# Optimization experiments

Measured on AMD Instinct MI355X. Metric: run time of the kernel, lower is better.

Reference implementation:

```python
import jax, jax.numpy as jnp
import numpy as np

EPS = 1e-5


def setup_inputs() -> dict:
    key = jax.random.key(0)
    ks = jax.random.split(key, 8)
    B, S, D, H, IN, OUT = 4096, 128, 64, 256, 8192, 1
    s = lambda n: 1.0 / np.sqrt(n)
    return {
        "x": jax.random.normal(ks[0], (B, IN), dtype=jnp.float32),
        "gamma": jnp.ones((IN,), jnp.float32),
        "beta": jnp.zeros((IN,), jnp.float32),
        "W_in": jax.random.normal(ks[1], (IN, IN), jnp.float32) * s(IN),
        "W_ih": jax.random.normal(ks[2], (4 * H, D), jnp.float32) * s(H),
        "b_ih": jnp.zeros((4 * H,), jnp.float32),
        "W_hh": jax.random.normal(ks[3], (4 * H, H), jnp.float32) * s(H),
        "b_hh": jnp.zeros((4 * H,), jnp.float32),
        "W_ta": jax.random.normal(ks[4], (S, S * H), jnp.float32) * s(S * H),
        "b_ta": jnp.zeros((S,), jnp.float32),
        "W_out": jax.random.normal(ks[5], (OUT, H), jnp.float32) * s(H),
    }


def _ta_lstm(x, gamma, beta, W_in, W_ih, b_ih, W_hh, b_hh, W_ta, b_ta, W_out):
    B, IN = x.shape
    H4 = W_hh.shape[0]
    H = H4 // 4
    S = W_ta.shape[0]
    D = IN // S

    # BatchNorm1d (training mode: batch statistics, biased variance)
    mean = jnp.mean(x, axis=0)
    var = jnp.mean(jnp.square(x - mean), axis=0)
    xn = (x - mean) * jax.lax.rsqrt(var + EPS) * gamma + beta

    # layer_in (no bias)
    proj = xn @ W_in.T  # [B, IN]

    # precompute input-side gate activations for all timesteps at once
    xs = proj.reshape(B, S, D)  # time-major column blocks
    gates_x = jnp.einsum("bsd,gd->sbg", xs, W_ih) + b_ih + b_hh  # [S, B, 4H]

    def step(carry, gx):
        h, c = carry
        gates = gx + h @ W_hh.T  # [B, 4H]
        i, f, g, o = jnp.split(gates, 4, axis=-1)
        i = jax.nn.sigmoid(i)
        f = jax.nn.sigmoid(f)
        g = jnp.tanh(g)
        o = jax.nn.sigmoid(o)
        c = f * c + i * g
        h = o * jnp.tanh(c)
        return (h, c), h

    h0 = jnp.zeros((B, H), x.dtype)
    c0 = jnp.zeros((B, H), x.dtype)
    _, hs = jax.lax.scan(step, (h0, c0), gates_x)  # hs: [S, B, H]

    hs_bsh = jnp.transpose(hs, (1, 0, 2))  # [B, S, H]
    total_ht = hs_bsh.reshape(B, S * H)  # matches torch.cat over time

    # temporal attention: relu -> softmax over last dim
    beta_t = jax.nn.softmax(jax.nn.relu(total_ht @ W_ta.T + b_ta), axis=-1)  # [B, S]

    pooled = jnp.einsum("bsh,bs->bh", hs_bsh, beta_t)  # [B, H]
    return pooled @ W_out.T  # [B, out_dim]


def reference(x, gamma, beta, W_in, W_ih, b_ih, W_hh, b_hh, W_ta, b_ta, W_out):
    return _ta_lstm(x, gamma, beta, W_in, W_ih, b_ih, W_hh, b_hh, W_ta, b_ta, W_out)
```

## Files before the change

kernel.cpp:

```cpp
#include <hip/hip_runtime.h>
#include <hip/hip_bf16.h>

#define BB 4096
#define INF 8192
#define SS 128
#define HH 256

typedef __attribute__((ext_vector_type(8))) short short8;
typedef __attribute__((ext_vector_type(4))) float f32x4;

__device__ __forceinline__ float sigm(float x) { return 1.f / (1.f + __expf(-x)); }
__device__ __forceinline__ float tanh_fast(float x) {
    float cx = fminf(15.f, fmaxf(-15.f, x));
    float e = __expf(2.f * cx);
    return (e - 1.f) / (e + 1.f);
}
__device__ __forceinline__ unsigned short f2bf(float f) {
    __hip_bfloat16 b = __float2bfloat16(f);
    return *(unsigned short*)&b;
}
__device__ __forceinline__ float bf2f(unsigned short u) {
    __hip_bfloat16 b = *(__hip_bfloat16*)&u;
    return __bfloat162float(b);
}

#define GLD(g, l) __builtin_amdgcn_global_load_lds(                              \
        (const __attribute__((address_space(1))) void*)(g),                      \
        (__attribute__((address_space(3))) void*)(l), 16, 0, 0)

__global__ __launch_bounds__(256) void bn_partial(const float* __restrict__ x,
                                                  float* __restrict__ colsum,
                                                  float* __restrict__ colsumsq) {
    int j = blockIdx.x * 256 + threadIdx.x;
    int r0 = blockIdx.y * 256;
    float s1 = 0.f, s2 = 0.f;
    for (int r = r0; r < r0 + 256; ++r) {
        float v = x[(size_t)r * INF + j];
        s1 += v;
        s2 += v * v;
    }
    atomicAdd(&colsum[j], s1);
    atomicAdd(&colsumsq[j], s2);
}

__global__ __launch_bounds__(256) void bn_finalize(const float* __restrict__ colsum,
                                                   const float* __restrict__ colsumsq,
                                                   const float* __restrict__ gamma,
                                                   const float* __restrict__ beta,
                                                   float* __restrict__ scl,
                                                   float* __restrict__ shf) {
    int j = blockIdx.x * 256 + threadIdx.x;
    float mean = colsum[j] * (1.f / BB);
    float var = colsumsq[j] * (1.f / BB) - mean * mean;
    float a = gamma[j] * rsqrtf(var + 1e-5f);
    scl[j] = a;
    shf[j] = beta[j] - mean * a;
}

__global__ __launch_bounds__(256) void split_x(const float* __restrict__ x,
                                               const float* __restrict__ scl,
                                               const float* __restrict__ shf,
                                               unsigned short* __restrict__ hi,
                                               unsigned short* __restrict__ lo) {
    size_t i = ((size_t)blockIdx.x * 256 + threadIdx.x) * 4;
    float4 v = *(const float4*)(x + i);
    int col = (int)(i & (INF - 1));
    float4 s = *(const float4*)(scl + col);
    float4 h = *(const float4*)(shf + col);
    float f[4] = {fmaf(v.x, s.x, h.x), fmaf(v.y, s.y, h.y),
                  fmaf(v.z, s.z, h.z), fmaf(v.w, s.w, h.w)};
    ushort4 hv, lv;
    unsigned short* hp = (unsigned short*)&hv;
    unsigned short* lp = (unsigned short*)&lv;
#pragma unroll
    for (int k = 0; k < 4; ++k) {
        unsigned short hb = f2bf(f[k]);
        hp[k] = hb;
        lp[k] = f2bf(f[k] - bf2f(hb));
    }
    *(ushort4*)(hi + i) = hv;
    *(ushort4*)(lo + i) = lv;
}

__global__ __launch_bounds__(256) void split_w(const float* __restrict__ w,
                                               unsigned short* __restrict__ hi,
                                               unsigned short* __restrict__ lo) {
    size_t i = ((size_t)blockIdx.x * 256 + threadIdx.x) * 4;
    float4 v = *(const float4*)(w + i);
    float f[4] = {v.x, v.y, v.z, v.w};
    ushort4 hv, lv;
    unsigned short* hp = (unsigned short*)&hv;
    unsigned short* lp = (unsigned short*)&lv;
#pragma unroll
    for (int k = 0; k < 4; ++k) {
        unsigned short hb = f2bf(f[k]);
        hp[k] = hb;
        lp[k] = f2bf(f[k] - bf2f(hb));
    }
    *(ushort4*)(hi + i) = hv;
    *(ushort4*)(lo + i) = lv;
}

__global__ __launch_bounds__(128) void pack_w(const float* __restrict__ Wih,
                                              const float* __restrict__ Whh,
                                              const float* __restrict__ bih,
                                              const float* __restrict__ bhh,
                                              unsigned short* __restrict__ Wch,
                                              unsigned short* __restrict__ Wcl,
                                              float* __restrict__ biascat) {
    int r = blockIdx.x;
    int c = r >> 2, g = r & 3;
    int t = threadIdx.x;
    if (t == 0) biascat[r] = bih[g * 256 + c] + bhh[g * 256 + c];
    if (t >= 80) return;
    float4 v;
    if (t < 16)
        v = *(const float4*)(Wih + (size_t)(g * 256 + c) * 64 + t * 4);
    else
        v = *(const float4*)(Whh + (size_t)(g * 256 + c) * 256 + (t - 16) * 4);
    float f[4] = {v.x, v.y, v.z, v.w};
    ushort4 hv, lv;
    unsigned short* hp = (unsigned short*)&hv;
    unsigned short* lp = (unsigned short*)&lv;
#pragma unroll
    for (int k = 0; k < 4; ++k) {
        unsigned short hb = f2bf(f[k]);
        hp[k] = hb;
        lp[k] = f2bf(f[k] - bf2f(hb));
    }
    *(ushort4*)(Wch + (size_t)r * 320 + t * 4) = hv;
    *(ushort4*)(Wcl + (size_t)r * 320 + t * 4) = lv;
}

__global__ __launch_bounds__(256) void gemm_mfma_split(
    const unsigned short* __restrict__ Ah, const unsigned short* __restrict__ Al,
    const unsigned short* __restrict__ Bh, const unsigned short* __restrict__ Bl,
    unsigned short* __restrict__ projsplit, int K) {
    __shared__ unsigned short AsH[4096], AsL[4096], BsH[4096], BsL[4096];
    const int tid = threadIdx.x;
    const int lane = tid & 63, wid = tid >> 6;
    int bid = blockIdx.x;
    int grp = bid >> 8, loc = bid & 255;
    int bx = ((grp & 3) << 4) | (loc & 15);
    int by = ((grp >> 2) << 4) | (loc >> 4);
    const int row0 = by << 7, col0 = bx << 7;
    const int wm = (wid & 1) << 6, wn = (wid >> 1) << 6;
    const int q = lane >> 4, l15 = lane & 15;

    const int s0 = wid * 128 + lane, s1 = s0 + 64;
    const int r0 = s0 >> 2, k0 = (((s0 & 3) ^ ((r0 >> 1) & 3)) << 3);
    const int r1 = s1 >> 2, k1 = (((s1 & 3) ^ ((r1 >> 1) & 3)) << 3);
    const size_t aoff0 = (size_t)(row0 + r0) * K + k0;
    const size_t aoff1 = (size_t)(row0 + r1) * K + k1;
    const size_t boff0 = (size_t)(col0 + r0) * K + k0;
    const size_t boff1 = (size_t)(col0 + r1) * K + k1;
    const int lb0 = (wid * 128) * 8, lb1 = lb0 + 512;

    f32x4 acc[4][4];
#pragma unroll
    for (int i = 0; i < 4; ++i)
#pragma unroll
        for (int j = 0; j < 4; ++j) acc[i][j] = (f32x4){0.f, 0.f, 0.f, 0.f};

    for (int kb = 0; kb < K; kb += 32) {
        __syncthreads();
        GLD(Ah + aoff0 + kb, &AsH[lb0]);
        GLD(Ah + aoff1 + kb, &AsH[lb1]);
        GLD(Al + aoff0 + kb, &AsL[lb0]);
        GLD(Al + aoff1 + kb, &AsL[lb1]);
        GLD(Bh + boff0 + kb, &BsH[lb0]);
        GLD(Bh + boff1 + kb, &BsH[lb1]);
        GLD(Bl + boff0 + kb, &BsL[lb0]);
        GLD(Bl + boff1 + kb, &BsL[lb1]);
        __syncthreads();

        short8 ahf[4], alf[4], bhf[4], blf[4];
#pragma unroll
        for (int i = 0; i < 4; ++i) {
            int ra = wm + i * 16 + l15;
            int offa = ra * 32 + ((q ^ ((ra >> 1) & 3)) << 3);
            ahf[i] = *(const short8*)&AsH[offa];
            alf[i] = *(const short8*)&AsL[offa];
            int rb = wn + i * 16 + l15;
            int offb = rb * 32 + ((q ^ ((rb >> 1) & 3)) << 3);
            bhf[i] = *(const short8*)&BsH[offb];
            blf[i] = *(const short8*)&BsL[offb];
        }
#pragma unroll
        for (int i = 0; i < 4; ++i)
#pragma unroll
            for (int j = 0; j < 4; ++j) {
                acc[i][j] = __builtin_amdgcn_mfma_f32_16x16x32_bf16(ahf[i], bhf[j], acc[i][j], 0, 0, 0);
                acc[i][j] = __builtin_amdgcn_mfma_f32_16x16x32_bf16(ahf[i], blf[j], acc[i][j], 0, 0, 0);
                acc[i][j] = __builtin_amdgcn_mfma_f32_16x16x32_bf16(alf[i], bhf[j], acc[i][j], 0, 0, 0);
            }
    }

#pragma unroll
    for (int i = 0; i < 4; ++i)
#pragma unroll
        for (int j = 0; j < 4; ++j) {
            int col = col0 + wn + j * 16 + l15;
            int slice = col >> 6, c6 = col & 63;
            unsigned short* ps = projsplit + (size_t)slice * 524288;
#pragma unroll
            for (int r = 0; r < 4; ++r) {
                int row = row0 + wm + i * 16 + q * 4 + r;
                float v = acc[i][j][r];
                unsigned short hb = f2bf(v);
                ps[row * 64 + c6] = hb;
                ps[262144 + row * 64 + c6] = f2bf(v - bf2f(hb));
            }
        }
}

__global__ __launch_bounds__(256) void lstm_step_mfma(
    const unsigned short* __restrict__ projsplit,
    const unsigned short* __restrict__ Wch, const unsigned short* __restrict__ Wcl,
    const float* __restrict__ biascat,
    const unsigned short* __restrict__ hin_h, const unsigned short* __restrict__ hin_l,
    unsigned short* __restrict__ hout_h, unsigned short* __restrict__ hout_l,
    float* __restrict__ cbuf, float* __restrict__ hs, int s) {
    __shared__ unsigned short AsH[4096], AsL[4096], BsH[4096], BsL[4096];
    __shared__ float gates[128][132];
    __shared__ float sbias[128];
    const int tid = threadIdx.x;
    const int lane = tid & 63, wid = tid >> 6;
    const int row0 = (blockIdx.x & 31) << 7;
    const int col0 = (blockIdx.x >> 5) << 7;
    if (tid < 128) sbias[tid] = biascat[col0 + tid];

    const int wm = (wid & 1) << 6, wn = (wid >> 1) << 6;
    const int q = lane >> 4, l15 = lane & 15;
    const int s0 = wid * 128 + lane, s1 = s0 + 64;
    const int r0 = s0 >> 2, k0 = (((s0 & 3) ^ ((r0 >> 1) & 3)) << 3);
    const int r1 = s1 >> 2, k1 = (((s1 & 3) ^ ((r1 >> 1) & 3)) << 3);
    const int lb0 = (wid * 128) * 8, lb1 = lb0 + 512;

    const unsigned short* psl = projsplit + (size_t)s * 524288;

    f32x4 acc[4][4];
#pragma unroll
    for (int i = 0; i < 4; ++i)
#pragma unroll
        for (int j = 0; j < 4; ++j) acc[i][j] = (f32x4){0.f, 0.f, 0.f, 0.f};

    for (int kb = 0; kb < 10; ++kb) {
        __syncthreads();
        const unsigned short *pah0, *pal0, *pah1, *pal1;
        if (kb < 2) {
            int off0 = (row0 + r0) * 64 + kb * 32 + k0;
            int off1 = (row0 + r1) * 64 + kb * 32 + k1;
            pah0 = psl + off0;          pal0 = psl + 262144 + off0;
            pah1 = psl + off1;          pal1 = psl + 262144 + off1;
        } else {
            int kh = kb * 32 - 64;
            int off0 = (row0 + r0) * HH + kh + k0;
            int off1 = (row0 + r1) * HH + kh + k1;
            pah0 = hin_h + off0;        pal0 = hin_l + off0;
            pah1 = hin_h + off1;        pal1 = hin_l + off1;
        }
        const unsigned short* pbh0 = Wch + (size_t)(col0 + r0) * 320 + kb * 32 + k0;
        const unsigned short* pbh1 = Wch + (size_t)(col0 + r1) * 320 + kb * 32 + k1;
        const unsigned short* pbl0 = Wcl + (size_t)(col0 + r0) * 320 + kb * 32 + k0;
        const unsigned short* pbl1 = Wcl + (size_t)(col0 + r1) * 320 + kb * 32 + k1;
        GLD(pah0, &AsH[lb0]);
        GLD(pah1, &AsH[lb1]);
        GLD(pal0, &AsL[lb0]);
        GLD(pal1, &AsL[lb1]);
        GLD(pbh0, &BsH[lb0]);
        GLD(pbh1, &BsH[lb1]);
        GLD(pbl0, &BsL[lb0]);
        GLD(pbl1, &BsL[lb1]);
        __syncthreads();

        short8 ahf[4], alf[4], bhf[4], blf[4];
#pragma unroll
        for (int i = 0; i < 4; ++i) {
            int ra = wm + i * 16 + l15;
            int offa = ra * 32 + ((q ^ ((ra >> 1) & 3)) << 3);
            ahf[i] = *(const short8*)&AsH[offa];
            alf[i] = *(const short8*)&AsL[offa];
            int rb = wn + i * 16 + l15;
            int offb = rb * 32 + ((q ^ ((rb >> 1) & 3)) << 3);
            bhf[i] = *(const short8*)&BsH[offb];
            blf[i] = *(const short8*)&BsL[offb];
        }
#pragma unroll
        for (int i = 0; i < 4; ++i)
#pragma unroll
            for (int j = 0; j < 4; ++j) {
                acc[i][j] = __builtin_amdgcn_mfma_f32_16x16x32_bf16(ahf[i], bhf[j], acc[i][j], 0, 0, 0);
                acc[i][j] = __builtin_amdgcn_mfma_f32_16x16x32_bf16(ahf[i], blf[j], acc[i][j], 0, 0, 0);
                acc[i][j] = __builtin_amdgcn_mfma_f32_16x16x32_bf16(alf[i], bhf[j], acc[i][j], 0, 0, 0);
            }
    }

    __syncthreads();
#pragma unroll
    for (int i = 0; i < 4; ++i)
#pragma unroll
        for (int j = 0; j < 4; ++j)
#pragma unroll
            for (int r = 0; r < 4; ++r)
                gates[wm + i * 16 + q * 4 + r][wn + j * 16 + l15] = acc[i][j][r];
    __syncthreads();

    const int hc = tid & 31, rg = tid >> 5;
    const int hbase = col0 >> 2;
#pragma unroll
    for (int rr = 0; rr < 16; ++rr) {
        int row = rg * 16 + rr;
        int b = row0 + row;
        float4 g4 = *(const float4*)&gates[row][4 * hc];
        float4 b4 = *(const float4*)&sbias[4 * hc];
        size_t ci = (size_t)b * HH + hbase + hc;
        float cold = (s > 0) ? cbuf[ci] : 0.f;
        float i_ = sigm(g4.x + b4.x);
        float f_ = sigm(g4.y + b4.y);
        float g_ = tanh_fast(g4.z + b4.z);
        float o_ = sigm(g4.w + b4.w);
        float cn = fmaf(f_, cold, i_ * g_);
        float hn = o_ * tanh_fast(cn);
        cbuf[ci] = cn;
        hs[(size_t)s * (BB * HH) + ci] = hn;
        unsigned short hb = f2bf(hn);
        hout_h[ci] = hb;
        hout_l[ci] = f2bf(hn - bf2f(hb));
    }
}

__global__ __launch_bounds__(256) void q_kernel(const float* __restrict__ hs,
                                                const float* __restrict__ wout,
                                                float* __restrict__ q) {
    int wid = threadIdx.x >> 6, lane = threadIdx.x & 63;
    int p = (blockIdx.x << 2) + wid;
    int b = p & (BB - 1), s = p >> 12;
    const float* hp = hs + ((size_t)s * BB + b) * HH + (lane << 2);
    float4 h4 = *(const float4*)hp;
    float4 w4 = *(const float4*)(wout + (lane << 2));
    float v = h4.x * w4.x + h4.y * w4.y + h4.z * w4.z + h4.w * w4.w;
#pragma unroll
    for (int off = 32; off; off >>= 1) v += __shfl_xor(v, off);
    if (lane == 0) q[b * SS + s] = v;
}

__global__ __launch_bounds__(256) void attn_part(const float* __restrict__ hs,
                                                 const float* __restrict__ Wta,
                                                 float* __restrict__ part) {
    __shared__ float As[16][68];
    __shared__ float Bs[16][132];
    const int tid = threadIdx.x;
    const int tx = tid & 15, ty = tid >> 4;
    const int row0 = blockIdx.x << 6;
    const int jc = blockIdx.y;
    const int lrA = tid >> 2, lkA = (tid & 3) << 2;
    const int lrB = tid >> 1, lkB = (tid & 1) << 3;

    float acc[4][8];
#pragma unroll
    for (int i = 0; i < 4; ++i)
#pragma unroll
        for (int j = 0; j < 8; ++j) acc[i][j] = 0.f;

    for (int kb = 0; kb < 256; ++kb) {
        int k0 = (jc << 12) + (kb << 4);
        int sidx = k0 >> 8, h0 = k0 & 255;
        float4 av = *(const float4*)(hs + ((size_t)sidx * BB + row0 + lrA) * HH + h0 + lkA);
        const float* wp = Wta + (size_t)lrB * (SS * HH) + k0 + lkB;
        float4 bv0 = *(const float4*)wp;
        float4 bv1 = *(const float4*)(wp + 4);
        __syncthreads();
        As[lkA + 0][lrA] = av.x;
        As[lkA + 1][lrA] = av.y;
        As[lkA + 2][lrA] = av.z;
        As[lkA + 3][lrA] = av.w;
        Bs[lkB + 0][lrB] = bv0.x;
        Bs[lkB + 1][lrB] = bv0.y;
        Bs[lkB + 2][lrB] = bv0.z;
        Bs[lkB + 3][lrB] = bv0.w;
        Bs[lkB + 4][lrB] = bv1.x;
        Bs[lkB + 5][lrB] = bv1.y;
        Bs[lkB + 6][lrB] = bv1.z;
        Bs[lkB + 7][lrB] = bv1.w;
        __syncthreads();
#pragma unroll
        for (int k = 0; k < 16; ++k) {
            float4 af = *(const float4*)&As[k][ty << 2];
            float4 b0 = *(const float4*)&Bs[k][tx << 2];
            float4 b1 = *(const float4*)&Bs[k][64 + (tx << 2)];
            float ar[4] = {af.x, af.y, af.z, af.w};
            float br[8] = {b0.x, b0.y, b0.z, b0.w, b1.x, b1.y, b1.z, b1.w};
#pragma unroll
            for (int i = 0; i < 4; ++i)
#pragma unroll
                for (int j = 0; j < 8; ++j)
                    acc[i][j] = fmaf(ar[i], br[j], acc[i][j]);
        }
    }
#pragma unroll
    for (int i = 0; i < 4; ++i) {
        int b = row0 + (ty << 2) + i;
        float* pp = part + ((size_t)jc * BB + b) * SS;
        float4 o0 = {acc[i][0], acc[i][1], acc[i][2], acc[i][3]};
        float4 o1 = {acc[i][4], acc[i][5], acc[i][6], acc[i][7]};
        *(float4*)(pp + (tx << 2)) = o0;
        *(float4*)(pp + 64 + (tx << 2)) = o1;
    }
}

__global__ __launch_bounds__(256) void attn_finalize(const float* __restrict__ part,
                                                     const float* __restrict__ b_ta,
                                                     const float* __restrict__ q,
                                                     float* __restrict__ out) {
    int wid = threadIdx.x >> 6, lane = threadIdx.x & 63;
    int b = (blockIdx.x << 2) + wid;
    float l0 = b_ta[lane], l1 = b_ta[lane + 64];
#pragma unroll
    for (int j = 0; j < 8; ++j) {
        const float* pp = part + ((size_t)j * BB + b) * SS;
        l0 += pp[lane];
        l1 += pp[lane + 64];
    }
    l0 = fmaxf(l0, 0.f);
    l1 = fmaxf(l1, 0.f);
    float mx = fmaxf(l0, l1);
#pragma unroll
    for (int off = 32; off; off >>= 1) mx = fmaxf(mx, __shfl_xor(mx, off));
    float e0 = __expf(l0 - mx), e1 = __expf(l1 - mx);
    float num = fmaf(e0, q[b * SS + lane], e1 * q[b * SS + lane + 64]);
    float den = e0 + e1;
#pragma unroll
    for (int off = 32; off; off >>= 1) {
        num += __shfl_xor(num, off);
        den += __shfl_xor(den, off);
    }
    if (lane == 0) out[b] = num / den;
}

extern "C" void kernel_launch(void* const* d_in, const int* in_sizes, int n_in,
                              void* d_out, int out_size, void* d_ws, size_t ws_size,
                              hipStream_t stream) {
    const float* x     = (const float*)d_in[0];
    const float* gamma = (const float*)d_in[1];
    const float* beta_ = (const float*)d_in[2];
    const float* W_in  = (const float*)d_in[3];
    const float* W_ih  = (const float*)d_in[4];
    const float* b_ih  = (const float*)d_in[5];
    const float* W_hh  = (const float*)d_in[6];
    const float* b_hh  = (const float*)d_in[7];
    const float* W_ta  = (const float*)d_in[8];
    const float* b_ta  = (const float*)d_in[9];
    const float* W_out = (const float*)d_in[10];
    float* out = (float*)d_out;

    float* ws = (float*)d_ws;
    float* colsum   = ws;
    float* colsumsq = ws + 8192;
    float* scl      = ws + 16384;
    float* shf      = ws + 24576;
    float* biascat  = ws + 32768;
    float* qbuf     = ws + 33792;
    float* part     = ws + 558080;
    float* cbuf     = ws + 4752384;
    unsigned short* Wch   = (unsigned short*)(ws + 5800960);
    unsigned short* Wcl   = (unsigned short*)(ws + 5964800);
    unsigned short* hsp0h = (unsigned short*)(ws + 6128640);
    unsigned short* hsp0l = (unsigned short*)(ws + 6652928);
    unsigned short* hsp1h = (unsigned short*)(ws + 7177216);
    unsigned short* hsp1l = (unsigned short*)(ws + 7701504);
    float* hs = ws + 8388608;
    unsigned short* xh = (unsigned short*)hs;
    unsigned short* xl = xh + 33554432;
    unsigned short* Wh = xl + 33554432;
    unsigned short* Wl = Wh + 67108864;
    unsigned short* projsplit = (unsigned short*)(ws + 8388608 + 108003328);

    hipMemsetAsync(colsum, 0, 2 * 8192 * sizeof(float), stream);
    hipMemsetAsync(hsp0h, 0, 4194304, stream);

    bn_partial<<<dim3(32, 16), 256, 0, stream>>>(x, colsum, colsumsq);
    bn_finalize<<<32, 256, 0, stream>>>(colsum, colsumsq, gamma, beta_, scl, shf);
    split_x<<<32768, 256, 0, stream>>>(x, scl, shf, xh, xl);
    split_w<<<65536, 256, 0, stream>>>(W_in, Wh, Wl);
    pack_w<<<1024, 128, 0, stream>>>(W_ih, W_hh, b_ih, b_hh, Wch, Wcl, biascat);
    gemm_mfma_split<<<2048, 256, 0, stream>>>(xh, xl, Wh, Wl, projsplit, INF);
    for (int s = 0; s < 128; ++s) {
        const unsigned short* hih = (s & 1) ? hsp1h : hsp0h;
        const unsigned short* hil = (s & 1) ? hsp1l : hsp0l;
        unsigned short* hoh = (s & 1) ? hsp0h : hsp1h;
        unsigned short* hol = (s & 1) ? hsp0l : hsp1l;
        lstm_step_mfma<<<256, 256, 0, stream>>>(projsplit, Wch, Wcl, biascat,
                                                hih, hil, hoh, hol, cbuf, hs, s);
    }
    q_kernel<<<131072, 256, 0, stream>>>(hs, W_out, qbuf);
    attn_part<<<dim3(64, 8), 256, 0, stream>>>(hs, W_ta, part);
    attn_finalize<<<1024, 256, 0, stream>>>(part, b_ta, qbuf, out);
}
```

Before: 5.472 ms.

## Rewrite split-bf16 input GEMM as 256x256 tile kernel with 4-stage LDS ring pipeline

```diff
diff --git a/kernel.cpp b/kernel.cpp
--- a/kernel.cpp
+++ b/kernel.cpp
@@ -132,86 +132,152 @@
     *(ushort4*)(Wcl + (size_t)r * 320 + t * 4) = lv;
 }
 
-__global__ __launch_bounds__(256) void gemm_mfma_split(
+__global__ __launch_bounds__(512, 2) void gemm8(
     const unsigned short* __restrict__ Ah, const unsigned short* __restrict__ Al,
     const unsigned short* __restrict__ Bh, const unsigned short* __restrict__ Bl,
-    unsigned short* __restrict__ projsplit, int K) {
-    __shared__ unsigned short AsH[4096], AsL[4096], BsH[4096], BsL[4096];
+    unsigned short* __restrict__ projsplit) {
+    __shared__ unsigned short As[32768];
+    __shared__ unsigned short Bs[32768];
     const int tid = threadIdx.x;
     const int lane = tid & 63, wid = tid >> 6;
-    int bid = blockIdx.x;
-    int grp = bid >> 8, loc = bid & 255;
-    int bx = ((grp & 3) << 4) | (loc & 15);
-    int by = ((grp >> 2) << 4) | (loc >> 4);
-    const int row0 = by << 7, col0 = bx << 7;
-    const int wm = (wid & 1) << 6, wn = (wid >> 1) << 6;
-    const int q = lane >> 4, l15 = lane & 15;
-
-    const int s0 = wid * 128 + lane, s1 = s0 + 64;
-    const int r0 = s0 >> 2, k0 = (((s0 & 3) ^ ((r0 >> 1) & 3)) << 3);
-    const int r1 = s1 >> 2, k1 = (((s1 & 3) ^ ((r1 >> 1) & 3)) << 3);
-    const size_t aoff0 = (size_t)(row0 + r0) * K + k0;
-    const size_t aoff1 = (size_t)(row0 + r1) * K + k1;
-    const size_t boff0 = (size_t)(col0 + r0) * K + k0;
-    const size_t boff1 = (size_t)(col0 + r1) * K + k1;
-    const int lb0 = (wid * 128) * 8, lb1 = lb0 + 512;
-
-    f32x4 acc[4][4];
+    const int wmi = wid >> 2, wni = wid & 3;
+    const int l15 = lane & 15, q = lane >> 4;
+
+    const int bid = blockIdx.x;
+    const int wg = ((bid & 7) << 6) | (bid >> 3);
+    const int bx = wg >> 4, by = wg & 15;
+    const int row0 = by << 8, col0 = bx << 8;
+
+    const int slot = (tid & 7) ^ ((tid >> 3) & 7);
+    const int rr = ((tid >> 3) << 1) | (slot >> 2);
+    const int kgo = (slot & 3) << 3;
+    const int wbase = wid << 9;
+
+    const int dsb = ((l15 >> 1) << 6) + (((q | ((l15 & 1) << 2)) ^ (l15 >> 1)) << 3);
+
+#define STAGE_A(srcp, ks, ring)                                                   \
+    do {                                                                          \
+        const unsigned short* _g = (srcp) + (size_t)(row0 + rr) * INF + (ks) + kgo; \
+        GLD(_g, &As[((ring) << 13) + wbase]);                                     \
+        GLD(_g + (size_t)128 * INF, &As[((ring) << 13) + 4096 + wbase]);          \
+    } while (0)
+#define STAGE_B(srcp, ks, ring)                                                   \
+    do {                                                                          \
+        const unsigned short* _g = (srcp) + (size_t)(col0 + rr) * INF + (ks) + kgo; \
+        GLD(_g, &Bs[((ring) << 13) + wbase]);                                     \
+        GLD(_g + (size_t)128 * INF, &Bs[((ring) << 13) + 4096 + wbase]);          \
+    } while (0)
+#define LDA4(d, i2, rgofs)                                                        \
+    do {                                                                          \
+        d[0] = *(const short8*)&As[(rgofs) + wmi * 4096 + (i2)*2048 + 0 * 512 + dsb]; \
+        d[1] = *(const short8*)&As[(rgofs) + wmi * 4096 + (i2)*2048 + 1 * 512 + dsb]; \
+        d[2] = *(const short8*)&As[(rgofs) + wmi * 4096 + (i2)*2048 + 2 * 512 + dsb]; \
+        d[3] = *(const short8*)&As[(rgofs) + wmi * 4096 + (i2)*2048 + 3 * 512 + dsb]; \
+    } while (0)
+#define LDB4(d, rgofs)                                                            \
+    do {                                                                          \
+        d[0] = *(const short8*)&Bs[(rgofs) + wni * 2048 + 0 * 512 + dsb];         \
+        d[1] = *(const short8*)&Bs[(rgofs) + wni * 2048 + 1 * 512 + dsb];         \
+        d[2] = *(const short8*)&Bs[(rgofs) + wni * 2048 + 2 * 512 + dsb];         \
+        d[3] = *(const short8*)&Bs[(rgofs) + wni * 2048 + 3 * 512 + dsb];         \
+    } while (0)
+#define MFMA16(accx)                                                              \
+    do {                                                                          \
+        __builtin_amdgcn_s_setprio(1);                                            \
+        _Pragma("unroll") for (int i_ = 0; i_ < 4; ++i_)                          \
+            _Pragma("unroll") for (int j_ = 0; j_ < 4; ++j_)                      \
+                accx[i_][j_] = __builtin_amdgcn_mfma_f32_16x16x32_bf16(           \
+                    a[i_], b[j_], accx[i_][j_], 0, 0, 0);                         \
+        __builtin_amdgcn_s_setprio(0);                                            \
+    } while (0)
+
+    f32x4 acc0[4][4], acc1[4][4];
 #pragma unroll
     for (int i = 0; i < 4; ++i)
 #pragma unroll
-        for (int j = 0; j < 4; ++j) acc[i][j] = (f32x4){0.f, 0.f, 0.f, 0.f};
-
-    for (int kb = 0; kb < K; kb += 32) {
-        __syncthreads();
-        GLD(Ah + aoff0 + kb, &AsH[lb0]);
-        GLD(Ah + aoff1 + kb, &AsH[lb1]);
-        GLD(Al + aoff0 + kb, &AsL[lb0]);
-        GLD(Al + aoff1 + kb, &AsL[lb1]);
-        GLD(Bh + boff0 + kb, &BsH[lb0]);
-        GLD(Bh + boff1 + kb, &BsH[lb1]);
-        GLD(Bl + boff0 + kb, &BsL[lb0]);
-        GLD(Bl + boff1 + kb, &BsL[lb1]);
-        __syncthreads();
-
-        short8 ahf[4], alf[4], bhf[4], blf[4];
-#pragma unroll
-        for (int i = 0; i < 4; ++i) {
-            int ra = wm + i * 16 + l15;
-            int offa = ra * 32 + ((q ^ ((ra >> 1) & 3)) << 3);
-            ahf[i] = *(const short8*)&AsH[offa];
-            alf[i] = *(const short8*)&AsL[offa];
-            int rb = wn + i * 16 + l15;
-            int offb = rb * 32 + ((q ^ ((rb >> 1) & 3)) << 3);
-            bhf[i] = *(const short8*)&BsH[offb];
-            blf[i] = *(const short8*)&BsL[offb];
+        for (int j = 0; j < 4; ++j) {
+            acc0[i][j] = (f32x4){0.f, 0.f, 0.f, 0.f};
+            acc1[i][j] = (f32x4){0.f, 0.f, 0.f, 0.f};
         }
-#pragma unroll
-        for (int i = 0; i < 4; ++i)
-#pragma unroll
-            for (int j = 0; j < 4; ++j) {
-                acc[i][j] = __builtin_amdgcn_mfma_f32_16x16x32_bf16(ahf[i], bhf[j], acc[i][j], 0, 0, 0);
-                acc[i][j] = __builtin_amdgcn_mfma_f32_16x16x32_bf16(ahf[i], blf[j], acc[i][j], 0, 0, 0);
-                acc[i][j] = __builtin_amdgcn_mfma_f32_16x16x32_bf16(alf[i], bhf[j], acc[i][j], 0, 0, 0);
-            }
+
+    short8 a[4], b[4];
+
+    STAGE_A(Ah, 0, 0);
+    STAGE_B(Bh, 0, 0);
+    STAGE_A(Al, 0, 1);
+    STAGE_B(Bh, 0, 1);
+    STAGE_A(Ah, 0, 2);
+    STAGE_B(Bl, 0, 2);
+    asm volatile("s_waitcnt vmcnt(8)" ::: "memory");
+    __builtin_amdgcn_s_barrier();
+
+    int seg3 = 0, ks3 = 32;
+    for (int t = 0; t < 765; ++t) {
+        const int rg = (t & 3) << 13;
+        const int sr = (t + 3) & 3;
+        const unsigned short* sA = (seg3 == 1) ? Al : Ah;
+        const unsigned short* sB = (seg3 == 2) ? Bl : Bh;
+        LDA4(a, 0, rg);
+        LDB4(b, rg);
+        STAGE_A(sA, ks3, sr);
+        __builtin_amdgcn_s_barrier();
+        asm volatile("s_waitcnt lgkmcnt(0)" ::: "memory");
+        __builtin_amdgcn_sched_barrier(0);
+        MFMA16(acc0);
+        __builtin_amdgcn_s_barrier();
+        LDA4(a, 1, rg);
+        STAGE_B(sB, ks3, sr);
+        __builtin_amdgcn_s_barrier();
+        asm volatile("s_waitcnt lgkmcnt(0)" ::: "memory");
+        __builtin_amdgcn_sched_barrier(0);
+        MFMA16(acc1);
+        asm volatile("s_waitcnt vmcnt(8)" ::: "memory");
+        __builtin_amdgcn_s_barrier();
+        if (++seg3 == 3) { seg3 = 0; ks3 += 32; }
+    }
+    asm volatile("s_waitcnt vmcnt(0)" ::: "memory");
+    __builtin_amdgcn_s_barrier();
+    for (int t = 765; t < 768; ++t) {
+        const int rg = (t & 3) << 13;
+        LDA4(a, 0, rg);
+        LDB4(b, rg);
+        asm volatile("s_waitcnt lgkmcnt(0)" ::: "memory");
+        __builtin_amdgcn_sched_barrier(0);
+        MFMA16(acc0);
+        __builtin_amdgcn_s_barrier();
+        LDA4(a, 1, rg);
+        asm volatile("s_waitcnt lgkmcnt(0)" ::: "memory");
+        __builtin_amdgcn_sched_barrier(0);
+        MFMA16(acc1);
+        __builtin_amdgcn_s_barrier();
     }
 
 #pragma unroll
     for (int i = 0; i < 4; ++i)
 #pragma unroll
         for (int j = 0; j < 4; ++j) {
-            int col = col0 + wn + j * 16 + l15;
+            int col = col0 + wni * 64 + j * 16 + l15;
             int slice = col >> 6, c6 = col & 63;
             unsigned short* ps = projsplit + (size_t)slice * 524288;
 #pragma unroll
             for (int r = 0; r < 4; ++r) {
-                int row = row0 + wm + i * 16 + q * 4 + r;
-                float v = acc[i][j][r];
+                int row = row0 + wmi * 128 + i * 16 + q * 4 + r;
+                float v = acc0[i][j][r];
                 unsigned short hb = f2bf(v);
+                ps[row * 64 + c6] = hb;
+                ps[262144 + row * 64 + c6] = f2bf(v - bf2f(hb));
+                row += 64;
+                v = acc1[i][j][r];
+                hb = f2bf(v);
                 ps[row * 64 + c6] = hb;
                 ps[262144 + row * 64 + c6] = f2bf(v - bf2f(hb));
             }
         }
+#undef STAGE_A
+#undef STAGE_B
+#undef LDA4
+#undef LDB4
+#undef MFMA16
 }
 
 __global__ __launch_bounds__(256) void lstm_step_mfma(
@@ -484,7 +550,7 @@
     split_x<<<32768, 256, 0, stream>>>(x, scl, shf, xh, xl);
     split_w<<<65536, 256, 0, stream>>>(W_in, Wh, Wl);
     pack_w<<<1024, 128, 0, stream>>>(W_ih, W_hh, b_ih, b_hh, Wch, Wcl, biascat);
-    gemm_mfma_split<<<2048, 256, 0, stream>>>(xh, xl, Wh, Wl, projsplit, INF);
+    gemm8<<<512, 512, 0, stream>>>(xh, xl, Wh, Wl, projsplit);
     for (int s = 0; s < 128; ++s) {
         const unsigned short* hih = (s & 1) ? hsp1h : hsp0h;
         const unsigned short* hil = (s & 1) ? hsp1l : hsp0l;
```

New measurement: 5.989 ms. 1.09x slower.

## Fuse LSTM timesteps into one persistent kernel with per-row-tile grid barriers

Applied to the files above, without the earlier changes.

```diff
diff --git a/kernel.cpp b/kernel.cpp
--- a/kernel.cpp
+++ b/kernel.cpp
@@ -214,120 +214,146 @@
         }
 }
 
-__global__ __launch_bounds__(256) void lstm_step_mfma(
+__global__ __launch_bounds__(256, 1) void lstm_seq(
     const unsigned short* __restrict__ projsplit,
     const unsigned short* __restrict__ Wch, const unsigned short* __restrict__ Wcl,
     const float* __restrict__ biascat,
-    const unsigned short* __restrict__ hin_h, const unsigned short* __restrict__ hin_l,
-    unsigned short* __restrict__ hout_h, unsigned short* __restrict__ hout_l,
-    float* __restrict__ cbuf, float* __restrict__ hs, int s) {
-    __shared__ unsigned short AsH[4096], AsL[4096], BsH[4096], BsL[4096];
-    __shared__ float gates[128][132];
-    __shared__ float sbias[128];
+    unsigned short* __restrict__ h0h, unsigned short* __restrict__ h0l,
+    unsigned short* __restrict__ h1h, unsigned short* __restrict__ h1l,
+    float* __restrict__ hs, int* __restrict__ bar) {
+    __shared__ unsigned short BsH[20480];
+    __shared__ unsigned short BsL[20480];
+    __shared__ float gates[256 * 68];
+    __shared__ float sbias[64];
+
     const int tid = threadIdx.x;
-    const int lane = tid & 63, wid = tid >> 6;
-    const int row0 = (blockIdx.x & 31) << 7;
-    const int col0 = (blockIdx.x >> 5) << 7;
-    if (tid < 128) sbias[tid] = biascat[col0 + tid];
-
-    const int wm = (wid & 1) << 6, wn = (wid >> 1) << 6;
-    const int q = lane >> 4, l15 = lane & 15;
-    const int s0 = wid * 128 + lane, s1 = s0 + 64;
-    const int r0 = s0 >> 2, k0 = (((s0 & 3) ^ ((r0 >> 1) & 3)) << 3);
-    const int r1 = s1 >> 2, k1 = (((s1 & 3) ^ ((r1 >> 1) & 3)) << 3);
-    const int lb0 = (wid * 128) * 8, lb1 = lb0 + 512;
-
-    const unsigned short* psl = projsplit + (size_t)s * 524288;
-
-    f32x4 acc[4][4];
-#pragma unroll
-    for (int i = 0; i < 4; ++i)
-#pragma unroll
-        for (int j = 0; j < 4; ++j) acc[i][j] = (f32x4){0.f, 0.f, 0.f, 0.f};
-
-    for (int kb = 0; kb < 10; ++kb) {
+    const int lane = tid & 63, w = tid >> 6;
+    const int l15 = lane & 15, q = lane >> 4, qk = q * 8;
+    const int bid = blockIdx.x;
+    const int rt = bid & 15, ct = bid >> 4;
+    int* cnt = bar + rt * 32;
+
+    for (int it = 0; it < 10; ++it) {
+        int idx = it * 256 + tid;
+        int gg = idx / 40, sl0 = idx - gg * 40;
+        int sl = (sl0 & 0x38) | ((sl0 ^ gg) & 7);
+        *(short8*)((char*)BsH + gg * 640 + sl * 16) =
+            *(const short8*)(Wch + (size_t)(ct * 64 + gg) * 320 + sl0 * 8);
+        *(short8*)((char*)BsL + gg * 640 + sl * 16) =
+            *(const short8*)(Wcl + (size_t)(ct * 64 + gg) * 320 + sl0 * 8);
+    }
+    if (tid < 64) sbias[tid] = biascat[ct * 64 + tid];
+    __syncthreads();
+
+    const int grow = rt * 256 + w * 64 + l15;
+    const int hc = tid & 15, rg4 = tid >> 4;
+    float c[16];
+#pragma unroll
+    for (int i = 0; i < 16; ++i) c[i] = 0.f;
+
+#define LOADA(buf, kb_)                                                          \
+    do {                                                                         \
+        _Pragma("unroll") for (int i_ = 0; i_ < 4; ++i_) {                       \
+            if ((kb_) < 2) {                                                     \
+                size_t o = (size_t)(grow + i_ * 16) * 64 + (kb_) * 32 + qk;      \
+                aH[buf][i_] = *(const short8*)(psh + o);                         \
+                aL[buf][i_] = *(const short8*)(psl2 + o);                        \
+            } else {                                                             \
+                size_t o = (size_t)(grow + i_ * 16) * 256 + ((kb_) * 32 - 64) + qk; \
+                aH[buf][i_] = *(const short8*)(hih + o);                         \
+                aL[buf][i_] = *(const short8*)(hil + o);                         \
+            }                                                                    \
+        }                                                                        \
+    } while (0)
+#define LOADB(buf, kb_)                                                          \
+    do {                                                                         \
+        _Pragma("unroll") for (int j_ = 0; j_ < 4; ++j_) {                       \
+            int gg = j_ * 16 + l15;                                              \
+            int slot = (kb_) * 4 + q;                                            \
+            int sl = (slot & 0x38) | ((slot ^ gg) & 7);                          \
+            int off = gg * 640 + sl * 16;                                        \
+            bH[buf][j_] = *(const short8*)((const char*)BsH + off);              \
+            bL[buf][j_] = *(const short8*)((const char*)BsL + off);              \
+        }                                                                        \
+    } while (0)
+
+    for (int s = 0; s < 128; ++s) {
+        const unsigned short* psh = projsplit + (size_t)s * 524288;
+        const unsigned short* psl2 = psh + 262144;
+        const unsigned short* hih = (s & 1) ? h1h : h0h;
+        const unsigned short* hil = (s & 1) ? h1l : h0l;
+        unsigned short* hoh = (s & 1) ? h0h : h1h;
+        unsigned short* hol = (s & 1) ? h0l : h1l;
+
+        f32x4 acc[4][4];
+#pragma unroll
+        for (int i = 0; i < 4; ++i)
+#pragma unroll
+            for (int j = 0; j < 4; ++j) acc[i][j] = (f32x4){0.f, 0.f, 0.f, 0.f};
+
+        short8 aH[2][4], aL[2][4], bH[2][4], bL[2][4];
+        LOADA(0, 0);
+        LOADA(1, 1);
+        LOADB(0, 0);
+#pragma unroll
+        for (int kb = 0; kb < 10; ++kb) {
+            const int cb = kb & 1, nb = cb ^ 1;
+            if (kb < 9) LOADB(nb, kb + 1);
+#pragma unroll
+            for (int i = 0; i < 4; ++i)
+#pragma unroll
+                for (int j = 0; j < 4; ++j) {
+                    acc[i][j] = __builtin_amdgcn_mfma_f32_16x16x32_bf16(aH[cb][i], bH[cb][j], acc[i][j], 0, 0, 0);
+                    acc[i][j] = __builtin_amdgcn_mfma_f32_16x16x32_bf16(aH[cb][i], bL[cb][j], acc[i][j], 0, 0, 0);
+                    acc[i][j] = __builtin_amdgcn_mfma_f32_16x16x32_bf16(aL[cb][i], bH[cb][j], acc[i][j], 0, 0, 0);
+                }
+            if (kb < 8) LOADA(cb, kb + 2);
+        }
+
+#pragma unroll
+        for (int i = 0; i < 4; ++i)
+#pragma unroll
+            for (int j = 0; j < 4; ++j)
+#pragma unroll
+                for (int r = 0; r < 4; ++r)
+                    gates[(w * 64 + i * 16 + q * 4 + r) * 68 + j * 16 + l15] = acc[i][j][r];
         __syncthreads();
-        const unsigned short *pah0, *pal0, *pah1, *pal1;
-        if (kb < 2) {
-            int off0 = (row0 + r0) * 64 + kb * 32 + k0;
-            int off1 = (row0 + r1) * 64 + kb * 32 + k1;
-            pah0 = psl + off0;          pal0 = psl + 262144 + off0;
-            pah1 = psl + off1;          pal1 = psl + 262144 + off1;
-        } else {
-            int kh = kb * 32 - 64;
-            int off0 = (row0 + r0) * HH + kh + k0;
-            int off1 = (row0 + r1) * HH + kh + k1;
-            pah0 = hin_h + off0;        pal0 = hin_l + off0;
-            pah1 = hin_h + off1;        pal1 = hin_l + off1;
+
+#pragma unroll
+        for (int rr = 0; rr < 16; ++rr) {
+            int row = rg4 * 16 + rr;
+            float4 g4 = *(const float4*)&gates[row * 68 + 4 * hc];
+            float4 b4 = *(const float4*)&sbias[4 * hc];
+            float i_ = sigm(g4.x + b4.x);
+            float f_ = sigm(g4.y + b4.y);
+            float g_ = tanh_fast(g4.z + b4.z);
+            float o_ = sigm(g4.w + b4.w);
+            float cn = fmaf(f_, c[rr], i_ * g_);
+            c[rr] = cn;
+            float hn = o_ * tanh_fast(cn);
+            size_t ci = (size_t)(rt * 256 + row) * HH + ct * 16 + hc;
+            hs[(size_t)s * (BB * HH) + ci] = hn;
+            unsigned short hb = f2bf(hn);
+            hoh[ci] = hb;
+            hol[ci] = f2bf(hn - bf2f(hb));
         }
-        const unsigned short* pbh0 = Wch + (size_t)(col0 + r0) * 320 + kb * 32 + k0;
-        const unsigned short* pbh1 = Wch + (size_t)(col0 + r1) * 320 + kb * 32 + k1;
-        const unsigned short* pbl0 = Wcl + (size_t)(col0 + r0) * 320 + kb * 32 + k0;
-        const unsigned short* pbl1 = Wcl + (size_t)(col0 + r1) * 320 + kb * 32 + k1;
-        GLD(pah0, &AsH[lb0]);
-        GLD(pah1, &AsH[lb1]);
-        GLD(pal0, &AsL[lb0]);
-        GLD(pal1, &AsL[lb1]);
-        GLD(pbh0, &BsH[lb0]);
-        GLD(pbh1, &BsH[lb1]);
-        GLD(pbl0, &BsL[lb0]);
-        GLD(pbl1, &BsL[lb1]);
+
         __syncthreads();
-
-        short8 ahf[4], alf[4], bhf[4], blf[4];
-#pragma unroll
-        for (int i = 0; i < 4; ++i) {
-            int ra = wm + i * 16 + l15;
-            int offa = ra * 32 + ((q ^ ((ra >> 1) & 3)) << 3);
-            ahf[i] = *(const short8*)&AsH[offa];
-            alf[i] = *(const short8*)&AsL[offa];
-            int rb = wn + i * 16 + l15;
-            int offb = rb * 32 + ((q ^ ((rb >> 1) & 3)) << 3);
-            bhf[i] = *(const short8*)&BsH[offb];
-            blf[i] = *(const short8*)&BsL[offb];
+        if (s < 127) {
+            if (tid == 0) {
+                __threadfence();
+                __hip_atomic_fetch_add(cnt, 1, __ATOMIC_RELEASE,
+                                       __HIP_MEMORY_SCOPE_AGENT);
+                int target = 16 * (s + 1);
+                while (__hip_atomic_load(cnt, __ATOMIC_ACQUIRE,
+                                         __HIP_MEMORY_SCOPE_AGENT) < target) {}
+                __threadfence();
+            }
+            __syncthreads();
         }
-#pragma unroll
-        for (int i = 0; i < 4; ++i)
-#pragma unroll
-            for (int j = 0; j < 4; ++j) {
-                acc[i][j] = __builtin_amdgcn_mfma_f32_16x16x32_bf16(ahf[i], bhf[j], acc[i][j], 0, 0, 0);
-                acc[i][j] = __builtin_amdgcn_mfma_f32_16x16x32_bf16(ahf[i], blf[j], acc[i][j], 0, 0, 0);
-                acc[i][j] = __builtin_amdgcn_mfma_f32_16x16x32_bf16(alf[i], bhf[j], acc[i][j], 0, 0, 0);
-            }
-    }
-
-    __syncthreads();
-#pragma unroll
-    for (int i = 0; i < 4; ++i)
-#pragma unroll
-        for (int j = 0; j < 4; ++j)
-#pragma unroll
-            for (int r = 0; r < 4; ++r)
-                gates[wm + i * 16 + q * 4 + r][wn + j * 16 + l15] = acc[i][j][r];
-    __syncthreads();
-
-    const int hc = tid & 31, rg = tid >> 5;
-    const int hbase = col0 >> 2;
-#pragma unroll
-    for (int rr = 0; rr < 16; ++rr) {
-        int row = rg * 16 + rr;
-        int b = row0 + row;
-        float4 g4 = *(const float4*)&gates[row][4 * hc];
-        float4 b4 = *(const float4*)&sbias[4 * hc];
-        size_t ci = (size_t)b * HH + hbase + hc;
-        float cold = (s > 0) ? cbuf[ci] : 0.f;
-        float i_ = sigm(g4.x + b4.x);
-        float f_ = sigm(g4.y + b4.y);
-        float g_ = tanh_fast(g4.z + b4.z);
-        float o_ = sigm(g4.w + b4.w);
-        float cn = fmaf(f_, cold, i_ * g_);
-        float hn = o_ * tanh_fast(cn);
-        cbuf[ci] = cn;
-        hs[(size_t)s * (BB * HH) + ci] = hn;
-        unsigned short hb = f2bf(hn);
-        hout_h[ci] = hb;
-        hout_l[ci] = f2bf(hn - bf2f(hb));
-    }
+    }
+#undef LOADA
+#undef LOADB
 }
 
 __global__ __launch_bounds__(256) void q_kernel(const float* __restrict__ hs,
@@ -462,7 +488,7 @@
     float* biascat  = ws + 32768;
     float* qbuf     = ws + 33792;
     float* part     = ws + 558080;
-    float* cbuf     = ws + 4752384;
+    int*   bar      = (int*)(ws + 4752384);
     unsigned short* Wch   = (unsigned short*)(ws + 5800960);
     unsigned short* Wcl   = (unsigned short*)(ws + 5964800);
     unsigned short* hsp0h = (unsigned short*)(ws + 6128640);
@@ -478,6 +504,7 @@
 
     hipMemsetAsync(colsum, 0, 2 * 8192 * sizeof(float), stream);
     hipMemsetAsync(hsp0h, 0, 4194304, stream);
+    hipMemsetAsync(bar, 0, 16 * 32 * sizeof(int), stream);
 
     bn_partial<<<dim3(32, 16), 256, 0, stream>>>(x, colsum, colsumsq);
     bn_finalize<<<32, 256, 0, stream>>>(colsum, colsumsq, gamma, beta_, scl, shf);
@@ -485,14 +512,8 @@
     split_w<<<65536, 256, 0, stream>>>(W_in, Wh, Wl);
     pack_w<<<1024, 128, 0, stream>>>(W_ih, W_hh, b_ih, b_hh, Wch, Wcl, biascat);
     gemm_mfma_split<<<2048, 256, 0, stream>>>(xh, xl, Wh, Wl, projsplit, INF);
-    for (int s = 0; s < 128; ++s) {
-        const unsigned short* hih = (s & 1) ? hsp1h : hsp0h;
-        const unsigned short* hil = (s & 1) ? hsp1l : hsp0l;
-        unsigned short* hoh = (s & 1) ? hsp0h : hsp1h;
-        unsigned short* hol = (s & 1) ? hsp0l : hsp1l;
-        lstm_step_mfma<<<256, 256, 0, stream>>>(projsplit, Wch, Wcl, biascat,
-                                                hih, hil, hoh, hol, cbuf, hs, s);
-    }
+    lstm_seq<<<256, 256, 0, stream>>>(projsplit, Wch, Wcl, biascat,
+                                      hsp0h, hsp0l, hsp1h, hsp1l, hs, bar);
     q_kernel<<<131072, 256, 0, stream>>>(hs, W_out, qbuf);
     attn_part<<<dim3(64, 8), 256, 0, stream>>>(hs, W_ta, part);
     attn_finalize<<<1024, 256, 0, stream>>>(part, b_ta, qbuf, out);
```

Result: slower. 8.010 ms (+46.4%).
